# Performance work log

Measured on AMD Instinct MI355X. Metric: run time of the kernel, lower is better.

Reference implementation:

```python
import jax, jax.numpy as jnp
import numpy as np

DIM = 1024      # feature_size
K = 128         # num_clusters
E = 2           # expansion
G = 8           # groups
ITERN = 3       # Newton-Schulz iterations
DG = E * DIM // G  # 256 per-group dim


def setup_inputs() -> dict:
    key = jax.random.key(0)
    ks = jax.random.split(key, 10)
    f32 = jnp.float32
    return {
        "x": jax.random.normal(ks[0], (32, DIM, 16, 8), dtype=f32),
        "centroids": jax.random.normal(ks[1], (K, DG), dtype=f32) * 0.05,
        "W_inp": jax.random.normal(ks[2], (E * DIM, DIM), dtype=f32) * 0.02,
        "b_inp": jax.random.normal(ks[3], (E * DIM,), dtype=f32) * 0.01,
        "W_g": jax.random.normal(ks[4], (G, E * DIM), dtype=f32) * 0.02,
        "b_g": jax.random.normal(ks[5], (G,), dtype=f32) * 0.01,
        "W_gk": jax.random.normal(ks[6], (G * K, E * DIM), dtype=f32) * 0.02,
        "b_gk": jax.random.normal(ks[7], (G * K,), dtype=f32) * 0.01,
        "W_f": jax.random.normal(ks[8], (1, K), dtype=f32) * 0.05,
        "b_f": jax.random.normal(ks[9], (1,), dtype=f32) * 0.01,
    }


def _covpool(v):
    # v: [bs, d, h, w] -> second-order pooling [bs, d, d]; x @ I_hat @ x^T == centered outer product / M
    bs, d = v.shape[0], v.shape[1]
    m = v.shape[2] * v.shape[3]
    v = v.reshape(bs, d, m)
    vc = v - v.mean(axis=2, keepdims=True)
    return jnp.einsum('bdm,bem->bde', vc, vc) / m


def _sqrtm_ns(cov, iter_n):
    # MPNCOV Newton-Schulz matrix square root (iter_n >= 2)
    d = cov.shape[1]
    I3 = 3.0 * jnp.eye(d, dtype=cov.dtype)[None]
    norm_a = jnp.trace(cov, axis1=1, axis2=2)[:, None, None]  # pre-normalization by trace
    A = cov / norm_a
    ZY = 0.5 * (I3 - A)
    Y = A @ ZY
    Z = ZY
    for _ in range(1, iter_n - 1):
        ZY = 0.5 * (I3 - Z @ Y)
        Y, Z = Y @ ZY, ZY @ Z
    ZY = 0.5 * (Y @ (I3 - Z @ Y))
    return ZY * jnp.sqrt(norm_a)


def _triuvec(cov):
    # row-major upper-triangular (incl. diagonal) vectorization, matching MPNCOV Triuvec
    d = cov.shape[1]
    r, c = np.triu_indices(d)
    return cov[:, r, c]


def reference(x, centroids, W_inp, b_inp, W_g, b_g, W_gk, b_gk, W_f, b_f):
    resolution = x.shape[-1]
    b8, C, H, W = x.shape
    bs = b8 // 8
    # [bs*8, C, H, W] -> [bs, M, N] with M = 8*H*W, N = C
    xt = x.reshape(bs, 8, C, H, W).transpose(0, 2, 1, 3, 4).reshape(bs, C, 8 * H * W)
    xt = jnp.transpose(xt, (0, 2, 1))
    M = xt.shape[1]
    # L2-normalize along feature dim (F.normalize eps clamp)
    xt = xt / jnp.maximum(jnp.linalg.norm(xt, axis=2, keepdims=True), 1e-12)
    h = xt @ W_inp.T + b_inp                               # [bs, M, E*N]
    alpha_g = jax.nn.sigmoid(h @ W_g.T + b_g)              # [bs, M, G]
    alpha_gk = jax.nn.softmax(h @ W_gk.T + b_gk, axis=1)   # NOTE: nn.Softmax(dim=1) -> over M
    alpha_gk = alpha_gk.reshape(bs, M, G, K)
    rx = h.reshape(bs, M, G, DG)                           # [bs, M, G, DG]
    w = alpha_g[..., None] * alpha_gk                      # [bs, M, G, K]
    # fused residual-weighted sum over M: sum_m w*(x - c) = (sum_m w*x) - (sum_m w)*c
    vlad = jnp.einsum('bmgk,bmgd->bgkd', w, rx) - w.sum(axis=1)[..., None] * centroids
    # learnable fusion over clusters K
    vf = jnp.einsum('bgkd,k->bgd', vlad, W_f[0]) + b_f[0]  # [bs, G, DG]
    vf = jnp.transpose(vf, (0, 2, 1))                      # [bs, DG, G]
    vf = vf.reshape(bs, DG, G // resolution, resolution)
    cov = _covpool(vf)
    cov = _sqrtm_ns(cov, ITERN)
    return _triuvec(cov)                                   # [bs, DG*(DG+1)//2]
```

## Files before the change

### kernel.cpp

```cpp
#include <hip/hip_runtime.h>
#include <math.h>

typedef float f32x4 __attribute__((ext_vector_type(4)));
typedef short bf16x8 __attribute__((ext_vector_type(8)));
typedef unsigned short u16;

__device__ __forceinline__ u16 f2bf(float f) {
    unsigned u = __builtin_bit_cast(unsigned, f);
    u += 0x7fff + ((u >> 16) & 1);
    return (u16)(u >> 16);
}
__device__ __forceinline__ float bf2f(u16 s) {
    unsigned v = ((unsigned)s) << 16;
    return __builtin_bit_cast(float, v);
}
__device__ __forceinline__ void gload16(const void* g, void* l) {
    __builtin_amdgcn_global_load_lds(
        (const __attribute__((address_space(1))) unsigned int*)g,
        (__attribute__((address_space(3))) unsigned int*)l, 16, 0, 0);
}

__global__ __launch_bounds__(256) void k_transpose_norm(const float* __restrict__ x,
                                                        u16* __restrict__ xtn) {
    int b8 = blockIdx.x;
    int hh = blockIdx.y;
    int tid = threadIdx.x;
    __shared__ float tile[8][1032];
    __shared__ float inv[8];
    const float* src = x + (size_t)b8 * 1024 * 128 + hh * 8;
    #pragma unroll
    for (int r = 0; r < 4; ++r) {
        int c = tid * 4 + r;
        const float* p = src + (size_t)c * 128;
        float4 v0 = *(const float4*)(p);
        float4 v1 = *(const float4*)(p + 4);
        tile[0][c] = v0.x; tile[1][c] = v0.y; tile[2][c] = v0.z; tile[3][c] = v0.w;
        tile[4][c] = v1.x; tile[5][c] = v1.y; tile[6][c] = v1.z; tile[7][c] = v1.w;
    }
    __syncthreads();
    int w = tid >> 5, j = tid & 31;
    float s = 0.f;
    #pragma unroll 8
    for (int i = 0; i < 32; ++i) { float v = tile[w][i * 32 + j]; s += v * v; }
    #pragma unroll
    for (int m = 16; m; m >>= 1) s += __shfl_xor(s, m);
    if (j == 0) inv[w] = 1.0f / fmaxf(sqrtf(s), 1e-12f);
    __syncthreads();
    int b = b8 >> 3, t = b8 & 7;
    int c0 = tid * 4;
    for (int w2 = 0; w2 < 8; ++w2) {
        int m = t * 128 + hh * 8 + w2;
        float sc = inv[w2];
        u16* dst = xtn + ((size_t)b * 1024 + m) * 1024;
        ushort4 o;
        o.x = f2bf(tile[w2][c0 + 0] * sc);
        o.y = f2bf(tile[w2][c0 + 1] * sc);
        o.z = f2bf(tile[w2][c0 + 2] * sc);
        o.w = f2bf(tile[w2][c0 + 3] * sc);
        *(ushort4*)(dst + c0) = o;
    }
}

__global__ __launch_bounds__(256) void k_prep(const float* __restrict__ Wgk,
                                              const float* __restrict__ Winp,
                                              u16* __restrict__ wgkb,
                                              u16* __restrict__ winpT) {
    int bid = blockIdx.x, tid = threadIdx.x;
    if (bid < 2048) {
        int i = (bid * 256 + tid) * 4;
        float4 v = *(const float4*)(Wgk + i);
        ushort4 o;
        o.x = f2bf(v.x); o.y = f2bf(v.y); o.z = f2bf(v.z); o.w = f2bf(v.w);
        *(ushort4*)(wgkb + i) = o;
    } else {
        int tb = bid - 2048;
        int er = tb & 31, cr = tb >> 5;
        __shared__ float tile[64][65];
        #pragma unroll
        for (int i = 0; i < 16; ++i) {
            int idx = tid + i * 256;
            int r = idx >> 6, c = idx & 63;
            tile[r][c] = Winp[(size_t)(er * 64 + r) * 1024 + cr * 64 + c];
        }
        __syncthreads();
        #pragma unroll
        for (int i = 0; i < 16; ++i) {
            int idx = tid + i * 256;
            int cc = idx >> 6, rr = idx & 63;
            winpT[(size_t)(cr * 64 + cc) * 2048 + er * 64 + rr] = f2bf(tile[rr][cc]);
        }
    }
}

template <int BM, int BN, int WC, int MODE>
__global__ __launch_bounds__(512) void k_mfma_gemm(
    const u16* __restrict__ A, const u16* __restrict__ B,
    float* __restrict__ Cf, u16* __restrict__ Cb,
    const float* __restrict__ bias, int Kld, int Kloop, int N,
    long long zA, long long zB, long long zC)
{
    constexpr int WR = 8 / WC;
    constexpr int WM = BM / WR;
    constexpr int WN = BN / WC;
    constexpr int MR = WM / 16;
    constexpr int NR = WN / 16;
    constexpr int QA = BM / 64;
    constexpr int QB = BN / 64;
    constexpr int S = QA + QB;
    __shared__ u16 As[2][BM * 64];
    __shared__ u16 Bs[2][BN * 64];
    int bz = blockIdx.z;
    A += (size_t)bz * zA; B += (size_t)bz * zB;
    int tid = threadIdx.x, lane = tid & 63, wave = tid >> 6;
    int wr = wave / WC, wc = wave % WC;
    int i0 = blockIdx.y * BM, j0 = blockIdx.x * BN;
    int fr = lane & 15, fg = lane >> 4;
    f32x4 acc[MR][NR] = {};

    int srcOff = ((tid & 7) ^ ((tid >> 3) & 7)) * 8;

    auto stage = [&](int buf, int t) {
        int kt = t * 64;
        #pragma unroll
        for (int q = 0; q < QA; ++q) {
            int row = (q * 512 + tid) >> 3;
            gload16(A + (size_t)(i0 + row) * Kld + kt + srcOff,
                    &As[buf][(q * 512 + wave * 64) * 8]);
        }
        #pragma unroll
        for (int q = 0; q < QB; ++q) {
            int row = (q * 512 + tid) >> 3;
            gload16(B + (size_t)(j0 + row) * Kld + kt + srcOff,
                    &Bs[buf][(q * 512 + wave * 64) * 8]);
        }
    };
    auto compute = [&](int buf) {
        #pragma unroll
        for (int h = 0; h < 2; ++h) {
            bf16x8 af[MR], bv[NR];
            #pragma unroll
            for (int mi = 0; mi < MR; ++mi) {
                int row = wr * WM + mi * 16 + fr;
                af[mi] = *(const bf16x8*)&As[buf][row * 64 + ((h * 4 + fg) ^ (fr & 7)) * 8];
            }
            #pragma unroll
            for (int ni = 0; ni < NR; ++ni) {
                int row = wc * WN + ni * 16 + fr;
                bv[ni] = *(const bf16x8*)&Bs[buf][row * 64 + ((h * 4 + fg) ^ (fr & 7)) * 8];
            }
            #pragma unroll
            for (int mi = 0; mi < MR; ++mi)
                #pragma unroll
                for (int ni = 0; ni < NR; ++ni)
                    acc[mi][ni] = __builtin_amdgcn_mfma_f32_16x16x32_bf16(
                        af[mi], bv[ni], acc[mi][ni], 0, 0, 0);
        }
    };

    int nk = Kloop >> 6;
    stage(0, 0);
    int cur = 0;
    for (int t = 0; t < nk; ++t) {
        if (t + 1 < nk) {
            stage(cur ^ 1, t + 1);
            if constexpr (S == 6)       asm volatile("s_waitcnt vmcnt(6)" ::: "memory");
            else if constexpr (S == 4)  asm volatile("s_waitcnt vmcnt(4)" ::: "memory");
            else                        asm volatile("s_waitcnt vmcnt(8)" ::: "memory");
        } else {
            asm volatile("s_waitcnt vmcnt(0)" ::: "memory");
        }
        __builtin_amdgcn_s_barrier();
        __builtin_amdgcn_sched_barrier(0);
        compute(cur);
        __builtin_amdgcn_s_barrier();
        cur ^= 1;
    }

    if (MODE >= 1) {
        #pragma unroll
        for (int ni = 0; ni < NR; ++ni) {
            int col = j0 + wc * WN + ni * 16 + fr;
            float bvv = (MODE == 1) ? bias[col] : 0.f;
            #pragma unroll
            for (int mi = 0; mi < MR; ++mi)
                #pragma unroll
                for (int r = 0; r < 4; ++r) {
                    int row = i0 + wr * WM + mi * 16 + fg * 4 + r;
                    Cb[(size_t)row * N + col] = f2bf(acc[mi][ni][r] + bvv);
                }
        }
    } else {
        float* C2 = Cf + (size_t)bz * zC;
        #pragma unroll
        for (int ni = 0; ni < NR; ++ni) {
            int col = j0 + wc * WN + ni * 16 + fr;
            #pragma unroll
            for (int mi = 0; mi < MR; ++mi)
                #pragma unroll
                for (int r = 0; r < 4; ++r) {
                    int row = i0 + wr * WM + mi * 16 + fg * 4 + r;
                    C2[(size_t)row * N + col] = acc[mi][ni][r];
                }
        }
    }
}

__global__ __launch_bounds__(256) void k_wcred(const float* __restrict__ wcp,
                                               u16* __restrict__ wcb) {
    int i = (blockIdx.x * 256 + threadIdx.x) * 4;
    float4 a = *(const float4*)(wcp + i);
    float4 b = *(const float4*)(wcp + 1048576 + i);
    float4 c = *(const float4*)(wcp + 2097152 + i);
    float4 d = *(const float4*)(wcp + 3145728 + i);
    ushort4 o;
    o.x = f2bf(a.x + b.x + c.x + d.x);
    o.y = f2bf(a.y + b.y + c.y + d.y);
    o.z = f2bf(a.z + b.z + c.z + d.z);
    o.w = f2bf(a.w + b.w + c.w + d.w);
    *(ushort4*)(wcb + i) = o;
}

__global__ __launch_bounds__(256) void k_wgeff(const float* __restrict__ Winp,
                                               const float* __restrict__ Wg,
                                               float* __restrict__ wgp) {
    int cs = blockIdx.x, es = blockIdx.y;
    int tid = threadIdx.x;
    __shared__ float wg_l[8][64];
    #pragma unroll
    for (int i = 0; i < 2; ++i) {
        int idx = tid + i * 256;
        wg_l[idx >> 6][idx & 63] = Wg[(size_t)(idx >> 6) * 2048 + es * 64 + (idx & 63)];
    }
    __syncthreads();
    int c = cs * 256 + tid;
    float acc[8] = {};
    #pragma unroll 4
    for (int e = 0; e < 64; ++e) {
        float v = Winp[(size_t)(es * 64 + e) * 1024 + c];
        #pragma unroll
        for (int g = 0; g < 8; ++g) acc[g] += wg_l[g][e] * v;
    }
    #pragma unroll
    for (int g = 0; g < 8; ++g) wgp[(size_t)es * 8192 + g * 1024 + c] = acc[g];
}

__global__ __launch_bounds__(256) void k_wgred(const float* __restrict__ wgp,
                                               const float* __restrict__ Wg,
                                               const float* __restrict__ binp,
                                               const float* __restrict__ bg,
                                               float* __restrict__ wge,
                                               float* __restrict__ cg) {
    int idx = blockIdx.x * 256 + threadIdx.x;
    float s = 0.f;
    for (int es = 0; es < 32; ++es) s += wgp[(size_t)es * 8192 + idx];
    wge[idx] = s;
    if (blockIdx.x == 0) {
        int g = threadIdx.x >> 5, sub = threadIdx.x & 31;
        float t = 0.f;
        for (int e = sub; e < 2048; e += 32) t += Wg[(size_t)g * 2048 + e] * binp[e];
        #pragma unroll
        for (int m = 16; m; m >>= 1) t += __shfl_xor(t, m);
        if (sub == 0) cg[g] = t + bg[g];
    }
}

__global__ __launch_bounds__(256) void k_agT(const u16* __restrict__ xtn,
                                             const float* __restrict__ wge,
                                             const float* __restrict__ cg,
                                             float* __restrict__ agT) {
    int b = blockIdx.x, ms = blockIdx.y;
    int tid = threadIdx.x, w = tid >> 6, lane = tid & 63;
    __shared__ float wgel[8192];
    __shared__ float cgl[8];
    #pragma unroll
    for (int i = 0; i < 8; ++i) {
        int idx = tid + i * 256;
        *(float4*)&wgel[idx * 4] = *(const float4*)&wge[idx * 4];
    }
    if (tid < 8) cgl[tid] = cg[tid];
    __syncthreads();
    for (int r = 0; r < 8; ++r) {
        int m = ms * 32 + w * 8 + r;
        const u16* xr = xtn + ((size_t)b * 1024 + m) * 1024;
        float acc[8] = {};
        #pragma unroll
        for (int i = 0; i < 2; ++i) {
            int c0 = i * 512 + lane * 8;
            bf16x8 hv = *(const bf16x8*)(xr + c0);
            float xf[8];
            #pragma unroll
            for (int j = 0; j < 8; ++j) xf[j] = bf2f((u16)hv[j]);
            #pragma unroll
            for (int g = 0; g < 8; ++g) {
                float4 wa = *(const float4*)&wgel[g * 1024 + c0];
                float4 wb = *(const float4*)&wgel[g * 1024 + c0 + 4];
                acc[g] += xf[0] * wa.x + xf[1] * wa.y + xf[2] * wa.z + xf[3] * wa.w
                        + xf[4] * wb.x + xf[5] * wb.y + xf[6] * wb.z + xf[7] * wb.w;
            }
        }
        #pragma unroll
        for (int g = 0; g < 8; ++g)
            #pragma unroll
            for (int off = 32; off; off >>= 1) acc[g] += __shfl_xor(acc[g], off);
        if (lane < 8)
            agT[((size_t)b * 8 + lane) * 1024 + m] =
                1.f / (1.f + expf(-(acc[lane] + cgl[lane])));
    }
}

__global__ __launch_bounds__(256) void k_smstat(const u16* __restrict__ lt,
                                                const float* __restrict__ agT,
                                                const float* __restrict__ Wf,
                                                float2* __restrict__ mxs,
                                                float* __restrict__ u) {
    int gk = blockIdx.x, b = blockIdx.y;
    int tid = threadIdx.x;
    const u16* row = lt + (size_t)gk * 4096 + b * 1024;
    int g = gk >> 7;
    const float* ag = agT + ((size_t)b * 8 + g) * 1024;
    __shared__ float red[4], red2[4], red3[4];
    ushort4 rv = *(const ushort4*)(row + tid * 4);
    float v0 = bf2f(rv.x), v1 = bf2f(rv.y), v2 = bf2f(rv.z), v3 = bf2f(rv.w);
    float mx = fmaxf(fmaxf(v0, v1), fmaxf(v2, v3));
    #pragma unroll
    for (int m = 32; m; m >>= 1) mx = fmaxf(mx, __shfl_xor(mx, m));
    if ((tid & 63) == 0) red[tid >> 6] = mx;
    __syncthreads();
    mx = fmaxf(fmaxf(red[0], red[1]), fmaxf(red[2], red[3]));
    float e0 = expf(v0 - mx), e1 = expf(v1 - mx), e2 = expf(v2 - mx), e3 = expf(v3 - mx);
    float4 a = *(const float4*)(ag + tid * 4);
    float s = e0 + e1 + e2 + e3;
    float sag = a.x * e0 + a.y * e1 + a.z * e2 + a.w * e3;
    #pragma unroll
    for (int m = 32; m; m >>= 1) { s += __shfl_xor(s, m); sag += __shfl_xor(sag, m); }
    if ((tid & 63) == 0) { red2[tid >> 6] = s; red3[tid >> 6] = sag; }
    __syncthreads();
    if (tid == 0) {
        float st = red2[0] + red2[1] + red2[2] + red2[3];
        float sa = red3[0] + red3[1] + red3[2] + red3[3];
        float invs = 1.f / st;
        mxs[gk * 4 + b] = make_float2(mx, invs);
        u[((size_t)b * 8 + g) * 128 + (gk & 127)] = Wf[gk & 127] * sa * invs;
    }
}

__global__ __launch_bounds__(256) void k_wf2(const u16* __restrict__ lt,
                                             const float2* __restrict__ mxs,
                                             const float* __restrict__ Wf,
                                             const float* __restrict__ agT,
                                             float* __restrict__ wf) {
    int ms = blockIdx.x, bg = blockIdx.y;
    int b = bg >> 3, g = bg & 7;
    int tid = threadIdx.x;
    __shared__ float c1[128], mxl[128];
    __shared__ float part[256];
    if (tid < 128) {
        float2 st = mxs[(g * 128 + tid) * 4 + b];
        mxl[tid] = st.x;
        c1[tid] = Wf[tid] * st.y;
    }
    __syncthreads();
    int ml = tid & 127, kh = tid >> 7;
    const u16* base = lt + (size_t)(g * 128 + kh * 64) * 4096 + b * 1024 + ms * 128;
    float acc = 0.f;
    #pragma unroll 4
    for (int k = 0; k < 64; ++k) {
        float v = bf2f(base[(size_t)k * 4096 + ml]);
        acc += c1[kh * 64 + k] * expf(v - mxl[kh * 64 + k]);
    }
    part[tid] = acc;
    __syncthreads();
    if (tid < 128) {
        float agv = agT[((size_t)b * 8 + g) * 1024 + ms * 128 + tid];
        wf[(size_t)bg * 1024 + ms * 128 + tid] = (part[tid] + part[tid + 128]) * agv;
    }
}

__global__ __launch_bounds__(256) void k_wfx(const u16* __restrict__ xtn,
                                             const float* __restrict__ wf,
                                             float* __restrict__ wfxp) {
    int cs = blockIdx.x, ms = blockIdx.y, b = blockIdx.z;
    int tid = threadIdx.x;
    __shared__ float wfl[8][128];
    #pragma unroll
    for (int i = 0; i < 4; ++i) {
        int idx = tid + i * 256;
        wfl[idx >> 7][idx & 127] = wf[((size_t)b * 8 + (idx >> 7)) * 1024 + ms * 128 + (idx & 127)];
    }
    __syncthreads();
    int c = cs * 256 + tid;
    float acc[8] = {};
    for (int m = 0; m < 128; ++m) {
        float xv = bf2f(xtn[((size_t)b * 1024 + ms * 128 + m) * 1024 + c]);
        #pragma unroll
        for (int g = 0; g < 8; ++g) acc[g] += wfl[g][m] * xv;
    }
    #pragma unroll
    for (int g = 0; g < 8; ++g)
        wfxp[(((size_t)ms * 4 + b) * 8 + g) * 1024 + c] = acc[g];
}

__global__ __launch_bounds__(256) void k_vfpart(const float* __restrict__ wfxp,
                                                const u16* __restrict__ winpT,
                                                const float* __restrict__ u,
                                                const float* __restrict__ cent,
                                                const float* __restrict__ binp,
                                                float* __restrict__ vfp) {
    int g = blockIdx.x, cs = blockIdx.y;
    int tid = threadIdx.x;
    if (cs < 8) {
        __shared__ float wfx_l[4][128];
        #pragma unroll
        for (int i = 0; i < 2; ++i) {
            int idx = tid + i * 256;
            int bb = idx >> 7, c2 = idx & 127;
            float s = 0.f;
            #pragma unroll
            for (int msq = 0; msq < 8; ++msq)
                s += wfxp[(((size_t)msq * 4 + bb) * 8 + g) * 1024 + cs * 128 + c2];
            wfx_l[bb][c2] = s;
        }
        __syncthreads();
        int d = tid;
        float acc[4] = {};
        for (int c2 = 0; c2 < 128; ++c2) {
            float wv = bf2f(winpT[(size_t)(cs * 128 + c2) * 2048 + g * 256 + d]);
            #pragma unroll
            for (int bb = 0; bb < 4; ++bb) acc[bb] += wfx_l[bb][c2] * wv;
        }
        #pragma unroll
        for (int bb = 0; bb < 4; ++bb)
            vfp[(((size_t)bb * 8 + g) * 9 + cs) * 256 + d] = acc[bb];
    } else {
        __shared__ float ul[4][128];
        __shared__ float swl[4];
        #pragma unroll
        for (int i = 0; i < 2; ++i) {
            int idx = tid + i * 256;
            ul[idx >> 7][idx & 127] = u[((size_t)(idx >> 7) * 8 + g) * 128 + (idx & 127)];
        }
        __syncthreads();
        if (tid < 4) {
            float s = 0.f;
            for (int k = 0; k < 128; ++k) s += ul[tid][k];
            swl[tid] = s;
        }
        __syncthreads();
        int d = tid;
        float acc[4] = {};
        for (int k = 0; k < 128; ++k) {
            float cv = cent[k * 256 + d];
            #pragma unroll
            for (int bb = 0; bb < 4; ++bb) acc[bb] -= ul[bb][k] * cv;
        }
        float bi = binp[g * 256 + d];
        #pragma unroll
        for (int bb = 0; bb < 4; ++bb)
            vfp[(((size_t)bb * 8 + g) * 9 + 8) * 256 + d] = acc[bb] + swl[bb] * bi;
    }
}

#define MM8(DST, P, Q) do { if (act) { float s_ = 0.f; \
    _Pragma("unroll") \
    for (int l_ = 0; l_ < 8; ++l_) s_ += P[ii][l_] * Q[l_][jj]; \
    DST[ii][jj] = s_; } __syncthreads(); } while (0)

__global__ __launch_bounds__(256) void k_finalize(const float* __restrict__ vfp,
                                                  const float* __restrict__ bf,
                                                  float* __restrict__ VcOut,
                                                  float* __restrict__ Wrow,
                                                  float* __restrict__ s0) {
    int b = blockIdx.x;
    int tid = threadIdx.x;
    __shared__ float Vl[256][9];
    __shared__ float red[256];
    __shared__ float Sm[8][8], W1[8][8], W2[8][8], YmL[8][8], ZmL[8][8], ZYL[8][8], FmL[8][8];
    int d = tid;
    float bfv = bf[0];
    float vfl[8];
    #pragma unroll
    for (int g = 0; g < 8; ++g) {
        float acc = 0.f;
        for (int mc = 0; mc < 9; ++mc)
            acc += vfp[(((size_t)b * 8 + g) * 9 + mc) * 256 + d];
        vfl[g] = acc + bfv;
    }
    float mean = 0.f;
    #pragma unroll
    for (int g = 0; g < 8; ++g) mean += vfl[g];
    mean *= 0.125f;
    float trp = 0.f;
    #pragma unroll
    for (int g = 0; g < 8; ++g) { float v = vfl[g] - mean; Vl[d][g] = v; trp += v * v; }
    red[tid] = trp;
    __syncthreads();
    for (int s = 128; s > 0; s >>= 1) { if (tid < s) red[tid] += red[tid + s]; __syncthreads(); }
    float tr = red[0] * 0.125f;
    bool act = tid < 64;
    int ii = (tid >> 3) & 7, jj = tid & 7;
    if (act) {
        float sv = 0.f;
        for (int dd = 0; dd < 256; ++dd) sv += Vl[dd][ii] * Vl[dd][jj];
        Sm[ii][jj] = sv / (8.f * tr);
    }
    __syncthreads();
    if (act) {
        YmL[ii][jj] = (ii == jj ? 1.5f : 0.f) - 0.5f * Sm[ii][jj];
        ZmL[ii][jj] = (ii == jj ? -0.5f : 0.f);
    }
    __syncthreads();
    float ya = 0.f, za = 1.5f;
    MM8(W1, Sm, YmL);
    MM8(W2, ZmL, W1);
    float pa = za * ya;
    if (act) ZYL[ii][jj] = -0.5f * (za * YmL[ii][jj] + ya * ZmL[ii][jj] + W2[ii][jj]);
    __syncthreads();
    float zya = 1.5f - 0.5f * pa;
    MM8(W1, Sm, ZYL);
    MM8(W2, YmL, W1);
    if (act) YmL[ii][jj] = ya * ZYL[ii][jj] + zya * YmL[ii][jj] + W2[ii][jj];
    __syncthreads();
    ya = ya * zya;
    MM8(W1, Sm, ZmL);
    MM8(W2, ZYL, W1);
    if (act) ZmL[ii][jj] = zya * ZmL[ii][jj] + za * ZYL[ii][jj] + W2[ii][jj];
    __syncthreads();
    za = zya * za;
    MM8(W1, Sm, YmL);
    MM8(W2, ZmL, W1);
    float p2a = za * ya;
    if (act) ZYL[ii][jj] = za * YmL[ii][jj] + ya * ZmL[ii][jj] + W2[ii][jj];
    __syncthreads();
    MM8(W1, Sm, ZYL);
    MM8(W2, YmL, W1);
    if (act) FmL[ii][jj] = 0.5f * ((3.f - p2a) * YmL[ii][jj] - ya * ZYL[ii][jj] - W2[ii][jj]);
    __syncthreads();
    float fa = 0.5f * ya * (3.f - p2a);
    float sqtr = sqrtf(tr);
    float scaleF = 1.f / (8.f * sqtr);
    #pragma unroll
    for (int jo = 0; jo < 8; ++jo) {
        float sv = 0.f;
        #pragma unroll
        for (int i = 0; i < 8; ++i) sv += Vl[d][i] * FmL[i][jo];
        Wrow[((size_t)b * 256 + d) * 8 + jo] = sv * scaleF;
    }
    #pragma unroll
    for (int jo = 0; jo < 8; ++jo) VcOut[((size_t)b * 256 + d) * 8 + jo] = Vl[d][jo];
    if (tid == 0) s0[b] = fa * sqtr;
}

__global__ __launch_bounds__(256) void k_output(const float* __restrict__ Vc,
                                                const float* __restrict__ Wrow,
                                                const float* __restrict__ s0,
                                                float* __restrict__ out) {
    int dd = blockIdx.x, b = blockIdx.y;
    int e = threadIdx.x;
    __shared__ float Vl[256][9];
    __shared__ float wr[8];
    float4 v0 = *(const float4*)(Vc + ((size_t)b * 256 + e) * 8);
    float4 v1 = *(const float4*)(Vc + ((size_t)b * 256 + e) * 8 + 4);
    Vl[e][0] = v0.x; Vl[e][1] = v0.y; Vl[e][2] = v0.z; Vl[e][3] = v0.w;
    Vl[e][4] = v1.x; Vl[e][5] = v1.y; Vl[e][6] = v1.z; Vl[e][7] = v1.w;
    if (e < 8) wr[e] = Wrow[((size_t)b * 256 + dd) * 8 + e];
    __syncthreads();
    if (e >= dd) {
        float v = (e == dd) ? s0[b] : 0.f;
        #pragma unroll
        for (int j = 0; j < 8; ++j) v += wr[j] * Vl[e][j];
        size_t idx = (size_t)b * 32896 + (size_t)dd * 256 - ((size_t)dd * (dd - 1)) / 2 + (e - dd);
        out[idx] = v;
    }
}

extern "C" void kernel_launch(void* const* d_in, const int* in_sizes, int n_in,
                              void* d_out, int out_size, void* d_ws, size_t ws_size,
                              hipStream_t stream) {
    const float* x    = (const float*)d_in[0];
    const float* cent = (const float*)d_in[1];
    const float* Winp = (const float*)d_in[2];
    const float* binp = (const float*)d_in[3];
    const float* Wg   = (const float*)d_in[4];
    const float* bg   = (const float*)d_in[5];
    const float* Wgk  = (const float*)d_in[6];
    const float* Wf   = (const float*)d_in[8];
    const float* bf   = (const float*)d_in[9];
    float* out = (float*)d_out;
    char* wsb = (char*)d_ws;

    u16*   xtnb  = (u16*)(wsb);
    u16*   ltb   = (u16*)(wsb + (8ull << 20));
    u16*   wgkb  = (u16*)(wsb + (16ull << 20));
    u16*   winpT = (u16*)(wsb + (20ull << 20));
    float* wcp   = (float*)(wsb + (24ull << 20));
    u16*   wcb   = (u16*)(wsb + (40ull << 20));
    float* misc  = (float*)(wsb + (42ull << 20));
    float* wgp   = misc;
    float* wge   = wgp + 262144;
    float* cg    = wge + 8192;
    float* agT   = cg + 8;
    float2* mxs  = (float2*)(agT + 32768);
    float* wf    = (float*)(mxs + 4096);
    float* u     = wf + 32768;
    float* wfxp  = u + 4096;
    float* vfp   = wfxp + 262144;
    float* Vc    = vfp + 73728;
    float* Wr    = Vc + 8192;
    float* s0    = Wr + 8192;

    k_transpose_norm<<<dim3(32, 16), 256, 0, stream>>>(x, xtnb);
    k_prep<<<2560, 256, 0, stream>>>(Wgk, Winp, wgkb, winpT);
    k_wgeff<<<dim3(4, 32), 256, 0, stream>>>(Winp, Wg, wgp);
    k_wgred<<<32, 256, 0, stream>>>(wgp, Wg, binp, bg, wge, cg);
    k_mfma_gemm<128, 128, 4, 0><<<dim3(8, 8, 4), 512, 0, stream>>>(
        wgkb, winpT, wcp, nullptr, nullptr, 2048, 512, 1024, 512LL, 512LL, 1048576LL);
    k_wcred<<<1024, 256, 0, stream>>>(wcp, wcb);
    k_mfma_gemm<128, 128, 4, 2><<<dim3(32, 8), 512, 0, stream>>>(
        wcb, xtnb, nullptr, ltb, nullptr, 1024, 1024, 4096, 0, 0, 0);
    k_agT<<<dim3(4, 32), 256, 0, stream>>>(xtnb, wge, cg, agT);
    k_smstat<<<dim3(1024, 4), 256, 0, stream>>>(ltb, agT, Wf, mxs, u);
    k_wf2<<<dim3(8, 32), 256, 0, stream>>>(ltb, mxs, Wf, agT, wf);
    k_wfx<<<dim3(4, 8, 4), 256, 0, stream>>>(xtnb, wf, wfxp);
    k_vfpart<<<dim3(8, 9), 256, 0, stream>>>(wfxp, winpT, u, cent, binp, vfp);
    k_finalize<<<4, 256, 0, stream>>>(vfp, bf, Vc, Wr, s0);
    k_output<<<dim3(256, 4), 256, 0, stream>>>(Vc, Wr, s0, out);
}
```

Baseline: 140.0 us.

## Fuse kernels, compute softmax stats in GEMM epilogue, widen K tile to 128

Merges the transpose/normalize, weight prep and gate-weight reduction into one launch, using atomics in place of a separate reduction pass. Fuses the wc reduction with the agT computation, and folds output writing into the finalize kernel. The logits GEMM epilogue now applies exp (without max subtraction) and atomically accumulates the softmax sums, which removes the separate stats kernel. The GEMM K-tile doubles to 128. Risks are overflow in the unshifted exp, nondeterministic float atomics, a doubled LDS footprint that may lower occupancy, and a 4-block final kernel that writes the whole output serially per row.

After: 157.5 us. 1.12x slower.

```diff
diff --git a/kernel.cpp b/kernel.cpp
--- a/kernel.cpp
+++ b/kernel.cpp
@@ -20,60 +20,62 @@
         (__attribute__((address_space(3))) unsigned int*)l, 16, 0, 0);
 }
 
-__global__ __launch_bounds__(256) void k_transpose_norm(const float* __restrict__ x,
-                                                        u16* __restrict__ xtn) {
-    int b8 = blockIdx.x;
-    int hh = blockIdx.y;
-    int tid = threadIdx.x;
-    __shared__ float tile[8][1032];
-    __shared__ float inv[8];
-    const float* src = x + (size_t)b8 * 1024 * 128 + hh * 8;
-    #pragma unroll
-    for (int r = 0; r < 4; ++r) {
-        int c = tid * 4 + r;
-        const float* p = src + (size_t)c * 128;
-        float4 v0 = *(const float4*)(p);
-        float4 v1 = *(const float4*)(p + 4);
-        tile[0][c] = v0.x; tile[1][c] = v0.y; tile[2][c] = v0.z; tile[3][c] = v0.w;
-        tile[4][c] = v1.x; tile[5][c] = v1.y; tile[6][c] = v1.z; tile[7][c] = v1.w;
-    }
-    __syncthreads();
-    int w = tid >> 5, j = tid & 31;
-    float s = 0.f;
-    #pragma unroll 8
-    for (int i = 0; i < 32; ++i) { float v = tile[w][i * 32 + j]; s += v * v; }
-    #pragma unroll
-    for (int m = 16; m; m >>= 1) s += __shfl_xor(s, m);
-    if (j == 0) inv[w] = 1.0f / fmaxf(sqrtf(s), 1e-12f);
-    __syncthreads();
-    int b = b8 >> 3, t = b8 & 7;
-    int c0 = tid * 4;
-    for (int w2 = 0; w2 < 8; ++w2) {
-        int m = t * 128 + hh * 8 + w2;
-        float sc = inv[w2];
-        u16* dst = xtn + ((size_t)b * 1024 + m) * 1024;
-        ushort4 o;
-        o.x = f2bf(tile[w2][c0 + 0] * sc);
-        o.y = f2bf(tile[w2][c0 + 1] * sc);
-        o.z = f2bf(tile[w2][c0 + 2] * sc);
-        o.w = f2bf(tile[w2][c0 + 3] * sc);
-        *(ushort4*)(dst + c0) = o;
-    }
-}
-
-__global__ __launch_bounds__(256) void k_prep(const float* __restrict__ Wgk,
-                                              const float* __restrict__ Winp,
-                                              u16* __restrict__ wgkb,
-                                              u16* __restrict__ winpT) {
+__global__ __launch_bounds__(256) void k_pre(const float* __restrict__ x,
+                                             const float* __restrict__ Wgk,
+                                             const float* __restrict__ Winp,
+                                             const float* __restrict__ Wg,
+                                             const float* __restrict__ binp,
+                                             const float* __restrict__ bg,
+                                             u16* __restrict__ xtn,
+                                             u16* __restrict__ wgkb,
+                                             u16* __restrict__ winpT,
+                                             float* __restrict__ wge,
+                                             float* __restrict__ cg) {
     int bid = blockIdx.x, tid = threadIdx.x;
-    if (bid < 2048) {
-        int i = (bid * 256 + tid) * 4;
+    if (bid < 512) {
+        int b8 = bid >> 4, hh = bid & 15;
+        __shared__ float tile[8][1032];
+        __shared__ float inv[8];
+        const float* src = x + (size_t)b8 * 1024 * 128 + hh * 8;
+        #pragma unroll
+        for (int r = 0; r < 4; ++r) {
+            int c = tid * 4 + r;
+            const float* p = src + (size_t)c * 128;
+            float4 v0 = *(const float4*)(p);
+            float4 v1 = *(const float4*)(p + 4);
+            tile[0][c] = v0.x; tile[1][c] = v0.y; tile[2][c] = v0.z; tile[3][c] = v0.w;
+            tile[4][c] = v1.x; tile[5][c] = v1.y; tile[6][c] = v1.z; tile[7][c] = v1.w;
+        }
+        __syncthreads();
+        int w = tid >> 5, j = tid & 31;
+        float s = 0.f;
+        #pragma unroll 8
+        for (int i = 0; i < 32; ++i) { float v = tile[w][i * 32 + j]; s += v * v; }
+        #pragma unroll
+        for (int m = 16; m; m >>= 1) s += __shfl_xor(s, m);
+        if (j == 0) inv[w] = 1.0f / fmaxf(sqrtf(s), 1e-12f);
+        __syncthreads();
+        int b = b8 >> 3, t = b8 & 7;
+        int c0 = tid * 4;
+        for (int w2 = 0; w2 < 8; ++w2) {
+            int m = t * 128 + hh * 8 + w2;
+            float sc = inv[w2];
+            u16* dst = xtn + ((size_t)b * 1024 + m) * 1024;
+            ushort4 o;
+            o.x = f2bf(tile[w2][c0 + 0] * sc);
+            o.y = f2bf(tile[w2][c0 + 1] * sc);
+            o.z = f2bf(tile[w2][c0 + 2] * sc);
+            o.w = f2bf(tile[w2][c0 + 3] * sc);
+            *(ushort4*)(dst + c0) = o;
+        }
+    } else if (bid < 2560) {
+        int i = ((bid - 512) * 256 + tid) * 4;
         float4 v = *(const float4*)(Wgk + i);
         ushort4 o;
         o.x = f2bf(v.x); o.y = f2bf(v.y); o.z = f2bf(v.z); o.w = f2bf(v.w);
         *(ushort4*)(wgkb + i) = o;
-    } else {
-        int tb = bid - 2048;
+    } else if (bid < 3072) {
+        int tb = bid - 2560;
         int er = tb & 31, cr = tb >> 5;
         __shared__ float tile[64][65];
         #pragma unroll
@@ -89,6 +91,37 @@
             int cc = idx >> 6, rr = idx & 63;
             winpT[(size_t)(cr * 64 + cc) * 2048 + er * 64 + rr] = f2bf(tile[rr][cc]);
         }
+    } else {
+        int t2 = bid - 3072;
+        int cs = t2 & 3, es = t2 >> 2;
+        __shared__ float wg_l[8][64];
+        #pragma unroll
+        for (int i = 0; i < 2; ++i) {
+            int idx = tid + i * 256;
+            wg_l[idx >> 6][idx & 63] = Wg[(size_t)(idx >> 6) * 2048 + es * 64 + (idx & 63)];
+        }
+        __syncthreads();
+        int c = cs * 256 + tid;
+        float acc[8] = {};
+        #pragma unroll 4
+        for (int e = 0; e < 64; ++e) {
+            float v = Winp[(size_t)(es * 64 + e) * 1024 + c];
+            #pragma unroll
+            for (int g = 0; g < 8; ++g) acc[g] += wg_l[g][e] * v;
+        }
+        #pragma unroll
+        for (int g = 0; g < 8; ++g) atomicAdd(&wge[g * 1024 + c], acc[g]);
+        if (cs == 0) {
+            int g = tid >> 5, sub = tid & 31;
+            float t = 0.f;
+            for (int e = sub; e < 64; e += 32) t += wg_l[g][e] * binp[es * 64 + e];
+            #pragma unroll
+            for (int m = 16; m; m >>= 1) t += __shfl_xor(t, m);
+            if (sub == 0) {
+                if (es == 0) t += bg[g];
+                atomicAdd(&cg[g], t);
+            }
+        }
     }
 }
 
@@ -96,7 +129,8 @@
 __global__ __launch_bounds__(512) void k_mfma_gemm(
     const u16* __restrict__ A, const u16* __restrict__ B,
     float* __restrict__ Cf, u16* __restrict__ Cb,
-    const float* __restrict__ bias, int Kld, int Kloop, int N,
+    const float* __restrict__ agT, float* __restrict__ ssum, float* __restrict__ sagm,
+    int Kld, int Kloop, int N,
     long long zA, long long zB, long long zC)
 {
     constexpr int WR = 8 / WC;
@@ -104,11 +138,11 @@
     constexpr int WN = BN / WC;
     constexpr int MR = WM / 16;
     constexpr int NR = WN / 16;
-    constexpr int QA = BM / 64;
-    constexpr int QB = BN / 64;
+    constexpr int QA = (BM * 128) / 4096;
+    constexpr int QB = (BN * 128) / 4096;
     constexpr int S = QA + QB;
-    __shared__ u16 As[2][BM * 64];
-    __shared__ u16 Bs[2][BN * 64];
+    __shared__ u16 As[2][BM * 128];
+    __shared__ u16 Bs[2][BN * 128];
     int bz = blockIdx.z;
     A += (size_t)bz * zA; B += (size_t)bz * zB;
     int tid = threadIdx.x, lane = tid & 63, wave = tid >> 6;
@@ -117,36 +151,36 @@
     int fr = lane & 15, fg = lane >> 4;
     f32x4 acc[MR][NR] = {};
 
-    int srcOff = ((tid & 7) ^ ((tid >> 3) & 7)) * 8;
+    int srcOff = ((tid & 15) ^ ((tid >> 4) & 7)) * 8;
 
     auto stage = [&](int buf, int t) {
-        int kt = t * 64;
+        int kt = t * 128;
         #pragma unroll
         for (int q = 0; q < QA; ++q) {
-            int row = (q * 512 + tid) >> 3;
+            int row = (q * 512 + tid) >> 4;
             gload16(A + (size_t)(i0 + row) * Kld + kt + srcOff,
                     &As[buf][(q * 512 + wave * 64) * 8]);
         }
         #pragma unroll
         for (int q = 0; q < QB; ++q) {
-            int row = (q * 512 + tid) >> 3;
+            int row = (q * 512 + tid) >> 4;
             gload16(B + (size_t)(j0 + row) * Kld + kt + srcOff,
                     &Bs[buf][(q * 512 + wave * 64) * 8]);
         }
     };
     auto compute = [&](int buf) {
         #pragma unroll
-        for (int h = 0; h < 2; ++h) {
+        for (int h = 0; h < 4; ++h) {
             bf16x8 af[MR], bv[NR];
             #pragma unroll
             for (int mi = 0; mi < MR; ++mi) {
                 int row = wr * WM + mi * 16 + fr;
-                af[mi] = *(const bf16x8*)&As[buf][row * 64 + ((h * 4 + fg) ^ (fr & 7)) * 8];
+                af[mi] = *(const bf16x8*)&As[buf][row * 128 + (((h * 4 + fg) ^ (fr & 7)) * 8)];
             }
             #pragma unroll
             for (int ni = 0; ni < NR; ++ni) {
                 int row = wc * WN + ni * 16 + fr;
-                bv[ni] = *(const bf16x8*)&Bs[buf][row * 64 + ((h * 4 + fg) ^ (fr & 7)) * 8];
+                bv[ni] = *(const bf16x8*)&Bs[buf][row * 128 + (((h * 4 + fg) ^ (fr & 7)) * 8)];
             }
             #pragma unroll
             for (int mi = 0; mi < MR; ++mi)
@@ -157,15 +191,15 @@
         }
     };
 
-    int nk = Kloop >> 6;
+    int nk = Kloop >> 7;
     stage(0, 0);
     int cur = 0;
     for (int t = 0; t < nk; ++t) {
         if (t + 1 < nk) {
             stage(cur ^ 1, t + 1);
-            if constexpr (S == 6)       asm volatile("s_waitcnt vmcnt(6)" ::: "memory");
-            else if constexpr (S == 4)  asm volatile("s_waitcnt vmcnt(4)" ::: "memory");
-            else                        asm volatile("s_waitcnt vmcnt(8)" ::: "memory");
+            if constexpr (S == 8)      asm volatile("s_waitcnt vmcnt(8)" ::: "memory");
+            else if constexpr (S == 6) asm volatile("s_waitcnt vmcnt(6)" ::: "memory");
+            else                       asm volatile("s_waitcnt vmcnt(4)" ::: "memory");
         } else {
             asm volatile("s_waitcnt vmcnt(0)" ::: "memory");
         }
@@ -176,19 +210,35 @@
         cur ^= 1;
     }
 
-    if (MODE >= 1) {
+    if constexpr (MODE == 3) {
+        int g = blockIdx.y;
+        int bcol = j0 >> 10;
+        float ag2[NR];
         #pragma unroll
         for (int ni = 0; ni < NR; ++ni) {
             int col = j0 + wc * WN + ni * 16 + fr;
-            float bvv = (MODE == 1) ? bias[col] : 0.f;
-            #pragma unroll
-            for (int mi = 0; mi < MR; ++mi)
-                #pragma unroll
-                for (int r = 0; r < 4; ++r) {
-                    int row = i0 + wr * WM + mi * 16 + fg * 4 + r;
-                    Cb[(size_t)row * N + col] = f2bf(acc[mi][ni][r] + bvv);
+            ag2[ni] = agT[((size_t)bcol * 8 + g) * 1024 + (col & 1023)];
+        }
+        #pragma unroll
+        for (int mi = 0; mi < MR; ++mi)
+            #pragma unroll
+            for (int r = 0; r < 4; ++r) {
+                int row = i0 + wr * WM + mi * 16 + fg * 4 + r;
+                float es = 0.f, sa = 0.f;
+                #pragma unroll
+                for (int ni = 0; ni < NR; ++ni) {
+                    int col = j0 + wc * WN + ni * 16 + fr;
+                    float e = expf(acc[mi][ni][r]);
+                    es += e; sa += ag2[ni] * e;
+                    Cb[(size_t)row * N + col] = f2bf(e - 1.f);
                 }
-        }
+                #pragma unroll
+                for (int m = 8; m; m >>= 1) { es += __shfl_xor(es, m); sa += __shfl_xor(sa, m); }
+                if (fr == 0) {
+                    atomicAdd(&ssum[row * 4 + bcol], es);
+                    atomicAdd(&sagm[row * 4 + bcol], sa);
+                }
+            }
     } else {
         float* C2 = Cf + (size_t)bz * zC;
         #pragma unroll
@@ -205,174 +255,106 @@
     }
 }
 
-__global__ __launch_bounds__(256) void k_wcred(const float* __restrict__ wcp,
-                                               u16* __restrict__ wcb) {
-    int i = (blockIdx.x * 256 + threadIdx.x) * 4;
-    float4 a = *(const float4*)(wcp + i);
-    float4 b = *(const float4*)(wcp + 1048576 + i);
-    float4 c = *(const float4*)(wcp + 2097152 + i);
-    float4 d = *(const float4*)(wcp + 3145728 + i);
-    ushort4 o;
-    o.x = f2bf(a.x + b.x + c.x + d.x);
-    o.y = f2bf(a.y + b.y + c.y + d.y);
-    o.z = f2bf(a.z + b.z + c.z + d.z);
-    o.w = f2bf(a.w + b.w + c.w + d.w);
-    *(ushort4*)(wcb + i) = o;
-}
-
-__global__ __launch_bounds__(256) void k_wgeff(const float* __restrict__ Winp,
-                                               const float* __restrict__ Wg,
-                                               float* __restrict__ wgp) {
-    int cs = blockIdx.x, es = blockIdx.y;
-    int tid = threadIdx.x;
-    __shared__ float wg_l[8][64];
-    #pragma unroll
-    for (int i = 0; i < 2; ++i) {
-        int idx = tid + i * 256;
-        wg_l[idx >> 6][idx & 63] = Wg[(size_t)(idx >> 6) * 2048 + es * 64 + (idx & 63)];
-    }
-    __syncthreads();
-    int c = cs * 256 + tid;
-    float acc[8] = {};
-    #pragma unroll 4
-    for (int e = 0; e < 64; ++e) {
-        float v = Winp[(size_t)(es * 64 + e) * 1024 + c];
-        #pragma unroll
-        for (int g = 0; g < 8; ++g) acc[g] += wg_l[g][e] * v;
-    }
-    #pragma unroll
-    for (int g = 0; g < 8; ++g) wgp[(size_t)es * 8192 + g * 1024 + c] = acc[g];
-}
-
-__global__ __launch_bounds__(256) void k_wgred(const float* __restrict__ wgp,
-                                               const float* __restrict__ Wg,
-                                               const float* __restrict__ binp,
-                                               const float* __restrict__ bg,
-                                               float* __restrict__ wge,
-                                               float* __restrict__ cg) {
-    int idx = blockIdx.x * 256 + threadIdx.x;
-    float s = 0.f;
-    for (int es = 0; es < 32; ++es) s += wgp[(size_t)es * 8192 + idx];
-    wge[idx] = s;
-    if (blockIdx.x == 0) {
-        int g = threadIdx.x >> 5, sub = threadIdx.x & 31;
-        float t = 0.f;
-        for (int e = sub; e < 2048; e += 32) t += Wg[(size_t)g * 2048 + e] * binp[e];
-        #pragma unroll
-        for (int m = 16; m; m >>= 1) t += __shfl_xor(t, m);
-        if (sub == 0) cg[g] = t + bg[g];
-    }
-}
-
-__global__ __launch_bounds__(256) void k_agT(const u16* __restrict__ xtn,
+__global__ __launch_bounds__(256) void k_mid(const float* __restrict__ wcp,
+                                             u16* __restrict__ wcb,
+                                             const u16* __restrict__ xtn,
                                              const float* __restrict__ wge,
                                              const float* __restrict__ cg,
                                              float* __restrict__ agT) {
-    int b = blockIdx.x, ms = blockIdx.y;
-    int tid = threadIdx.x, w = tid >> 6, lane = tid & 63;
-    __shared__ float wgel[8192];
-    __shared__ float cgl[8];
-    #pragma unroll
-    for (int i = 0; i < 8; ++i) {
-        int idx = tid + i * 256;
-        *(float4*)&wgel[idx * 4] = *(const float4*)&wge[idx * 4];
-    }
-    if (tid < 8) cgl[tid] = cg[tid];
-    __syncthreads();
-    for (int r = 0; r < 8; ++r) {
-        int m = ms * 32 + w * 8 + r;
-        const u16* xr = xtn + ((size_t)b * 1024 + m) * 1024;
-        float acc[8] = {};
-        #pragma unroll
-        for (int i = 0; i < 2; ++i) {
-            int c0 = i * 512 + lane * 8;
-            bf16x8 hv = *(const bf16x8*)(xr + c0);
-            float xf[8];
-            #pragma unroll
-            for (int j = 0; j < 8; ++j) xf[j] = bf2f((u16)hv[j]);
-            #pragma unroll
-            for (int g = 0; g < 8; ++g) {
-                float4 wa = *(const float4*)&wgel[g * 1024 + c0];
-                float4 wb = *(const float4*)&wgel[g * 1024 + c0 + 4];
-                acc[g] += xf[0] * wa.x + xf[1] * wa.y + xf[2] * wa.z + xf[3] * wa.w
-                        + xf[4] * wb.x + xf[5] * wb.y + xf[6] * wb.z + xf[7] * wb.w;
+    int bid = blockIdx.x, tid = threadIdx.x;
+    if (bid < 1024) {
+        int i = (bid * 256 + tid) * 4;
+        float4 a = *(const float4*)(wcp + i);
+        float4 b = *(const float4*)(wcp + 1048576 + i);
+        float4 c = *(const float4*)(wcp + 2097152 + i);
+        float4 d = *(const float4*)(wcp + 3145728 + i);
+        ushort4 o;
+        o.x = f2bf(a.x + b.x + c.x + d.x);
+        o.y = f2bf(a.y + b.y + c.y + d.y);
+        o.z = f2bf(a.z + b.z + c.z + d.z);
+        o.w = f2bf(a.w + b.w + c.w + d.w);
+        *(ushort4*)(wcb + i) = o;
+    } else {
+        int t2 = bid - 1024;
+        int b = t2 >> 5, ms = t2 & 31;
+        int w = tid >> 6, lane = tid & 63;
+        __shared__ float wgel[8192];
+        __shared__ float cgl[8];
+        #pragma unroll
+        for (int i = 0; i < 8; ++i) {
+            int idx = tid + i * 256;
+            *(float4*)&wgel[idx * 4] = *(const float4*)&wge[idx * 4];
+        }
+        if (tid < 8) cgl[tid] = cg[tid];
+        __syncthreads();
+        for (int r = 0; r < 8; ++r) {
+            int m = ms * 32 + w * 8 + r;
+            const u16* xr = xtn + ((size_t)b * 1024 + m) * 1024;
+            float acc[8] = {};
+            #pragma unroll
+            for (int i = 0; i < 2; ++i) {
+                int c0 = i * 512 + lane * 8;
+                bf16x8 hv = *(const bf16x8*)(xr + c0);
+                float xf[8];
+                #pragma unroll
+                for (int j = 0; j < 8; ++j) xf[j] = bf2f((u16)hv[j]);
+                #pragma unroll
+                for (int g = 0; g < 8; ++g) {
+                    float4 wa = *(const float4*)&wgel[g * 1024 + c0];
+                    float4 wb = *(const float4*)&wgel[g * 1024 + c0 + 4];
+                    acc[g] += xf[0] * wa.x + xf[1] * wa.y + xf[2] * wa.z + xf[3] * wa.w
+                            + xf[4] * wb.x + xf[5] * wb.y + xf[6] * wb.z + xf[7] * wb.w;
+                }
             }
-        }
-        #pragma unroll
-        for (int g = 0; g < 8; ++g)
-            #pragma unroll
-            for (int off = 32; off; off >>= 1) acc[g] += __shfl_xor(acc[g], off);
-        if (lane < 8)
-            agT[((size_t)b * 8 + lane) * 1024 + m] =
-                1.f / (1.f + expf(-(acc[lane] + cgl[lane])));
-    }
-}
-
-__global__ __launch_bounds__(256) void k_smstat(const u16* __restrict__ lt,
-                                                const float* __restrict__ agT,
-                                                const float* __restrict__ Wf,
-                                                float2* __restrict__ mxs,
-                                                float* __restrict__ u) {
-    int gk = blockIdx.x, b = blockIdx.y;
-    int tid = threadIdx.x;
-    const u16* row = lt + (size_t)gk * 4096 + b * 1024;
-    int g = gk >> 7;
-    const float* ag = agT + ((size_t)b * 8 + g) * 1024;
-    __shared__ float red[4], red2[4], red3[4];
-    ushort4 rv = *(const ushort4*)(row + tid * 4);
-    float v0 = bf2f(rv.x), v1 = bf2f(rv.y), v2 = bf2f(rv.z), v3 = bf2f(rv.w);
-    float mx = fmaxf(fmaxf(v0, v1), fmaxf(v2, v3));
-    #pragma unroll
-    for (int m = 32; m; m >>= 1) mx = fmaxf(mx, __shfl_xor(mx, m));
-    if ((tid & 63) == 0) red[tid >> 6] = mx;
-    __syncthreads();
-    mx = fmaxf(fmaxf(red[0], red[1]), fmaxf(red[2], red[3]));
-    float e0 = expf(v0 - mx), e1 = expf(v1 - mx), e2 = expf(v2 - mx), e3 = expf(v3 - mx);
-    float4 a = *(const float4*)(ag + tid * 4);
-    float s = e0 + e1 + e2 + e3;
-    float sag = a.x * e0 + a.y * e1 + a.z * e2 + a.w * e3;
-    #pragma unroll
-    for (int m = 32; m; m >>= 1) { s += __shfl_xor(s, m); sag += __shfl_xor(sag, m); }
-    if ((tid & 63) == 0) { red2[tid >> 6] = s; red3[tid >> 6] = sag; }
-    __syncthreads();
-    if (tid == 0) {
-        float st = red2[0] + red2[1] + red2[2] + red2[3];
-        float sa = red3[0] + red3[1] + red3[2] + red3[3];
-        float invs = 1.f / st;
-        mxs[gk * 4 + b] = make_float2(mx, invs);
-        u[((size_t)b * 8 + g) * 128 + (gk & 127)] = Wf[gk & 127] * sa * invs;
-    }
-}
-
-__global__ __launch_bounds__(256) void k_wf2(const u16* __restrict__ lt,
-                                             const float2* __restrict__ mxs,
+            #pragma unroll
+            for (int g = 0; g < 8; ++g)
+                #pragma unroll
+                for (int off = 32; off; off >>= 1) acc[g] += __shfl_xor(acc[g], off);
+            if (lane < 8)
+                agT[((size_t)b * 8 + lane) * 1024 + m] =
+                    1.f / (1.f + expf(-(acc[lane] + cgl[lane])));
+        }
+    }
+}
+
+__global__ __launch_bounds__(256) void k_wf2(const u16* __restrict__ em1,
+                                             const float* __restrict__ ssum,
+                                             const float* __restrict__ sagm,
                                              const float* __restrict__ Wf,
                                              const float* __restrict__ agT,
-                                             float* __restrict__ wf) {
+                                             float* __restrict__ wf, float* __restrict__ u) {
     int ms = blockIdx.x, bg = blockIdx.y;
     int b = bg >> 3, g = bg & 7;
     int tid = threadIdx.x;
-    __shared__ float c1[128], mxl[128];
+    __shared__ float c1[128];
     __shared__ float part[256];
+    __shared__ float c0s;
     if (tid < 128) {
-        float2 st = mxs[(g * 128 + tid) * 4 + b];
-        mxl[tid] = st.x;
-        c1[tid] = Wf[tid] * st.y;
-    }
-    __syncthreads();
+        int gk = g * 128 + tid;
+        float s = ssum[gk * 4 + b];
+        float wfk = Wf[tid];
+        float cv = wfk / s;
+        c1[tid] = cv;
+        part[tid] = cv;
+        if (ms == 0) u[bg * 128 + tid] = wfk * sagm[gk * 4 + b] / s;
+    } else part[tid] = 0.f;
+    __syncthreads();
+    for (int st = 128; st; st >>= 1) { if (tid < st) part[tid] += part[tid + st]; __syncthreads(); }
+    if (tid == 0) c0s = part[0];
+    __syncthreads();
+    float C0 = c0s;
     int ml = tid & 127, kh = tid >> 7;
-    const u16* base = lt + (size_t)(g * 128 + kh * 64) * 4096 + b * 1024 + ms * 128;
+    const u16* base = em1 + (size_t)(g * 128 + kh * 64) * 4096 + b * 1024 + ms * 128;
     float acc = 0.f;
     #pragma unroll 4
-    for (int k = 0; k < 64; ++k) {
-        float v = bf2f(base[(size_t)k * 4096 + ml]);
-        acc += c1[kh * 64 + k] * expf(v - mxl[kh * 64 + k]);
-    }
+    for (int k = 0; k < 64; ++k)
+        acc += c1[kh * 64 + k] * bf2f(base[(size_t)k * 4096 + ml]);
+    __syncthreads();
     part[tid] = acc;
     __syncthreads();
     if (tid < 128) {
         float agv = agT[((size_t)b * 8 + g) * 1024 + ms * 128 + tid];
-        wf[(size_t)bg * 1024 + ms * 128 + tid] = (part[tid] + part[tid + 128]) * agv;
+        wf[(size_t)bg * 1024 + ms * 128 + tid] = (C0 + part[tid] + part[tid + 128]) * agv;
     }
 }
 
@@ -465,17 +447,16 @@
     for (int l_ = 0; l_ < 8; ++l_) s_ += P[ii][l_] * Q[l_][jj]; \
     DST[ii][jj] = s_; } __syncthreads(); } while (0)
 
-__global__ __launch_bounds__(256) void k_finalize(const float* __restrict__ vfp,
-                                                  const float* __restrict__ bf,
-                                                  float* __restrict__ VcOut,
-                                                  float* __restrict__ Wrow,
-                                                  float* __restrict__ s0) {
+__global__ __launch_bounds__(256) void k_fin(const float* __restrict__ vfp,
+                                             const float* __restrict__ bf,
+                                             float* __restrict__ out) {
     int b = blockIdx.x;
-    int tid = threadIdx.x;
+    int tid = threadIdx.x, d = tid;
     __shared__ float Vl[256][9];
+    __shared__ float4 Vl4a[256], Vl4b[256];
     __shared__ float red[256];
+    __shared__ float Sp[4][64];
     __shared__ float Sm[8][8], W1[8][8], W2[8][8], YmL[8][8], ZmL[8][8], ZYL[8][8], FmL[8][8];
-    int d = tid;
     float bfv = bf[0];
     float vfl[8];
     #pragma unroll
@@ -491,18 +472,24 @@
     mean *= 0.125f;
     float trp = 0.f;
     #pragma unroll
-    for (int g = 0; g < 8; ++g) { float v = vfl[g] - mean; Vl[d][g] = v; trp += v * v; }
+    for (int g = 0; g < 8; ++g) { float v = vfl[g] - mean; Vl[d][g] = v; vfl[g] = v; trp += v * v; }
+    Vl4a[d] = make_float4(vfl[0], vfl[1], vfl[2], vfl[3]);
+    Vl4b[d] = make_float4(vfl[4], vfl[5], vfl[6], vfl[7]);
     red[tid] = trp;
     __syncthreads();
     for (int s = 128; s > 0; s >>= 1) { if (tid < s) red[tid] += red[tid + s]; __syncthreads(); }
     float tr = red[0] * 0.125f;
+    {
+        int q = tid >> 6, l = tid & 63;
+        int si = l >> 3, sj = l & 7;
+        float sv = 0.f;
+        for (int dd = q * 64; dd < q * 64 + 64; ++dd) sv += Vl[dd][si] * Vl[dd][sj];
+        Sp[q][l] = sv;
+    }
+    __syncthreads();
     bool act = tid < 64;
     int ii = (tid >> 3) & 7, jj = tid & 7;
-    if (act) {
-        float sv = 0.f;
-        for (int dd = 0; dd < 256; ++dd) sv += Vl[dd][ii] * Vl[dd][jj];
-        Sm[ii][jj] = sv / (8.f * tr);
-    }
+    if (act) Sm[ii][jj] = (Sp[0][tid] + Sp[1][tid] + Sp[2][tid] + Sp[3][tid]) / (8.f * tr);
     __syncthreads();
     if (act) {
         YmL[ii][jj] = (ii == jj ? 1.5f : 0.f) - 0.5f * Sm[ii][jj];
@@ -538,38 +525,22 @@
     float fa = 0.5f * ya * (3.f - p2a);
     float sqtr = sqrtf(tr);
     float scaleF = 1.f / (8.f * sqtr);
+    float wrj[8];
     #pragma unroll
     for (int jo = 0; jo < 8; ++jo) {
         float sv = 0.f;
         #pragma unroll
-        for (int i = 0; i < 8; ++i) sv += Vl[d][i] * FmL[i][jo];
-        Wrow[((size_t)b * 256 + d) * 8 + jo] = sv * scaleF;
-    }
-    #pragma unroll
-    for (int jo = 0; jo < 8; ++jo) VcOut[((size_t)b * 256 + d) * 8 + jo] = Vl[d][jo];
-    if (tid == 0) s0[b] = fa * sqtr;
-}
-
-__global__ __launch_bounds__(256) void k_output(const float* __restrict__ Vc,
-                                                const float* __restrict__ Wrow,
-                                                const float* __restrict__ s0,
-                                                float* __restrict__ out) {
-    int dd = blockIdx.x, b = blockIdx.y;
-    int e = threadIdx.x;
-    __shared__ float Vl[256][9];
-    __shared__ float wr[8];
-    float4 v0 = *(const float4*)(Vc + ((size_t)b * 256 + e) * 8);
-    float4 v1 = *(const float4*)(Vc + ((size_t)b * 256 + e) * 8 + 4);
-    Vl[e][0] = v0.x; Vl[e][1] = v0.y; Vl[e][2] = v0.z; Vl[e][3] = v0.w;
-    Vl[e][4] = v1.x; Vl[e][5] = v1.y; Vl[e][6] = v1.z; Vl[e][7] = v1.w;
-    if (e < 8) wr[e] = Wrow[((size_t)b * 256 + dd) * 8 + e];
-    __syncthreads();
-    if (e >= dd) {
-        float v = (e == dd) ? s0[b] : 0.f;
-        #pragma unroll
-        for (int j = 0; j < 8; ++j) v += wr[j] * Vl[e][j];
-        size_t idx = (size_t)b * 32896 + (size_t)dd * 256 - ((size_t)dd * (dd - 1)) / 2 + (e - dd);
-        out[idx] = v;
+        for (int i = 0; i < 8; ++i) sv += vfl[i] * FmL[i][jo];
+        wrj[jo] = sv * scaleF;
+    }
+    float s0v = fa * sqtr;
+    size_t base = (size_t)b * 32896 + (size_t)d * 256 - ((size_t)d * (d - 1)) / 2 - d;
+    for (int e = d; e < 256; ++e) {
+        float4 va = Vl4a[e], vb = Vl4b[e];
+        float v = wrj[0] * va.x + wrj[1] * va.y + wrj[2] * va.z + wrj[3] * va.w
+                + wrj[4] * vb.x + wrj[5] * vb.y + wrj[6] * vb.z + wrj[7] * vb.w;
+        if (e == d) v += s0v;
+        out[base + e] = v;
     }
 }
 
@@ -595,33 +566,27 @@
     float* wcp   = (float*)(wsb + (24ull << 20));
     u16*   wcb   = (u16*)(wsb + (40ull << 20));
     float* misc  = (float*)(wsb + (42ull << 20));
-    float* wgp   = misc;
-    float* wge   = wgp + 262144;
+    float* wge   = misc;
     float* cg    = wge + 8192;
-    float* agT   = cg + 8;
-    float2* mxs  = (float2*)(agT + 32768);
-    float* wf    = (float*)(mxs + 4096);
-    float* u     = wf + 32768;
-    float* wfxp  = u + 4096;
+    float* ssum  = cg + 8;
+    float* sagm  = ssum + 4096;
+    float* agT   = sagm + 4096;
+    float* u     = agT + 32768;
+    float* wf    = u + 4096;
+    float* wfxp  = wf + 32768;
     float* vfp   = wfxp + 262144;
-    float* Vc    = vfp + 73728;
-    float* Wr    = Vc + 8192;
-    float* s0    = Wr + 8192;
-
-    k_transpose_norm<<<dim3(32, 16), 256, 0, stream>>>(x, xtnb);
-    k_prep<<<2560, 256, 0, stream>>>(Wgk, Winp, wgkb, winpT);
-    k_wgeff<<<dim3(4, 32), 256, 0, stream>>>(Winp, Wg, wgp);
-    k_wgred<<<32, 256, 0, stream>>>(wgp, Wg, binp, bg, wge, cg);
+
+    hipMemsetAsync(misc, 0, 16392 * sizeof(float), stream);
+    k_pre<<<3200, 256, 0, stream>>>(x, Wgk, Winp, Wg, binp, bg, xtnb, wgkb, winpT, wge, cg);
     k_mfma_gemm<128, 128, 4, 0><<<dim3(8, 8, 4), 512, 0, stream>>>(
-        wgkb, winpT, wcp, nullptr, nullptr, 2048, 512, 1024, 512LL, 512LL, 1048576LL);
-    k_wcred<<<1024, 256, 0, stream>>>(wcp, wcb);
-    k_mfma_gemm<128, 128, 4, 2><<<dim3(32, 8), 512, 0, stream>>>(
-        wcb, xtnb, nullptr, ltb, nullptr, 1024, 1024, 4096, 0, 0, 0);
-    k_agT<<<dim3(4, 32), 256, 0, stream>>>(xtnb, wge, cg, agT);
-    k_smstat<<<dim3(1024, 4), 256, 0, stream>>>(ltb, agT, Wf, mxs, u);
-    k_wf2<<<dim3(8, 32), 256, 0, stream>>>(ltb, mxs, Wf, agT, wf);
+        wgkb, winpT, wcp, nullptr, nullptr, nullptr, nullptr,
+        2048, 512, 1024, 512LL, 512LL, 1048576LL);
+    k_mid<<<1152, 256, 0, stream>>>(wcp, wcb, xtnb, wge, cg, agT);
+    k_mfma_gemm<128, 128, 4, 3><<<dim3(32, 8, 1), 512, 0, stream>>>(
+        wcb, xtnb, nullptr, ltb, agT, ssum, sagm,
+        1024, 1024, 4096, 0, 0, 0);
+    k_wf2<<<dim3(8, 32), 256, 0, stream>>>(ltb, ssum, sagm, Wf, agT, wf, u);
     k_wfx<<<dim3(4, 8, 4), 256, 0, stream>>>(xtnb, wf, wfxp);
     k_vfpart<<<dim3(8, 9), 256, 0, stream>>>(wfxp, winpT, u, cent, binp, vfp);
-    k_finalize<<<4, 256, 0, stream>>>(vfp, bf, Vc, Wr, s0);
-    k_output<<<dim3(256, 4), 256, 0, stream>>>(Vc, Wr, s0, out);
-}
+    k_fin<<<4, 256, 0, stream>>>(vfp, bf, out);
+}
```
